# Kernel tuning notes

Hardware: AMD Instinct MI355X
Metric: run time of the kernel (lower is better)

## Reference

```python
import jax, jax.numpy as jnp
import numpy as np

N = 750_000      # total nodes (10,000 graphs x 75 superpixels)
E = 6_000_000    # directed edges (avg degree 8)
G = 10_000       # number of graphs
NINP, H, HFC, NCLS = 2, 64, 32, 10
BN_EPS = 1e-5


def setup_inputs() -> dict:
    key = jax.random.key(0)
    ks = jax.random.split(key, 12)
    x = jax.random.normal(ks[0], (N, NINP), dtype=jnp.float32)
    edge_index = jax.random.randint(ks[1], (2, E), 0, N, dtype=jnp.int32)
    batch = jnp.sort(jax.random.randint(ks[2], (N,), 0, G, dtype=jnp.int32))
    def glorot(k, shape):
        fan_in, fan_out = shape
        s = jnp.sqrt(6.0 / (fan_in + fan_out)).astype(jnp.float32)
        return jax.random.uniform(k, shape, jnp.float32, -s, s)
    return {
        "x": x, "edge_index": edge_index, "batch": batch,
        "W1": glorot(ks[3], (NINP, H)), "b1": jnp.zeros((H,), jnp.float32),
        "W2": glorot(ks[4], (H, H)),    "b2": jnp.zeros((H,), jnp.float32),
        "W3": glorot(ks[5], (H, H)),    "b3": jnp.zeros((H,), jnp.float32),
        "gamma": jnp.ones((H,), jnp.float32), "beta": jnp.zeros((H,), jnp.float32),
        "fcW1": glorot(ks[6], (H, HFC)),  "fcb1": jnp.zeros((HFC,), jnp.float32),
        "fcW2": glorot(ks[7], (HFC, NCLS)), "fcb2": jnp.zeros((NCLS,), jnp.float32),
    }


def reference(x, edge_index, batch, W1, b1, W2, b2, W3, b3,
              gamma, beta, fcW1, fcb1, fcW2, fcb2):
    n = x.shape[0]
    loop = jnp.arange(n, dtype=edge_index.dtype)
    src = jnp.concatenate([edge_index[0], loop])   # [E+N] self-loops added
    dst = jnp.concatenate([edge_index[1], loop])
    # symmetric GCN normalization: deg from destination with unit edge weights
    deg = jax.ops.segment_sum(jnp.ones_like(dst, jnp.float32), dst, num_segments=n)
    dinv = jnp.where(deg > 0, jax.lax.rsqrt(deg), 0.0)
    norm = (dinv[src] * dinv[dst])[:, None]        # [E+N, 1]

    def gcn_conv(h, W, b):
        h = h @ W                                   # linear transform first (small K)
        msg = h[src] * norm                         # gather + normalize
        return jax.ops.segment_sum(msg, dst, num_segments=n) + b  # scatter-add

    h = jax.nn.relu(gcn_conv(x, W1, b1))
    h = jax.nn.relu(gcn_conv(h, W2, b2))
    h = jax.nn.relu(gcn_conv(h, W3, b3))

    # global mean pool over graphs
    sums = jax.ops.segment_sum(h, batch, num_segments=G)
    cnts = jax.ops.segment_sum(jnp.ones((n, 1), jnp.float32), batch, num_segments=G)
    pooled = sums / jnp.maximum(cnts, 1.0)          # [G, H]

    # BatchNorm1d (training mode: batch statistics, biased variance)
    mean = pooled.mean(axis=0)
    var = pooled.var(axis=0)
    hbn = (pooled - mean) * jax.lax.rsqrt(var + BN_EPS) * gamma + beta

    h = jax.nn.relu(hbn @ fcW1 + fcb1)
    logits = h @ fcW2 + fcb2
    return jax.nn.log_softmax(logits, axis=1)
```

## Files before the change

kernel.cpp:

```cpp
#include <hip/hip_runtime.h>
#include <hip/hip_fp16.h>

#define HDIM 64
#define HFC 32
#define NCLS 10
#define DT32 32

#define NBUCK 256
#define BSH   12
#define BUCKN 4096
#define EPT   16
#define CHUNK 4096
#define CAPSH 16
#define CAP   (1 << CAPSH)

__device__ inline __half2 u2h2(unsigned int u) {
    __half2 r;
    *reinterpret_cast<unsigned int*>(&r) = u;
    return r;
}
__device__ inline unsigned int h22u(__half2 h) {
    return *reinterpret_cast<unsigned int*>(&h);
}

__device__ inline float fdot2u(unsigned int a, unsigned int b, float c) {
#if __has_builtin(__builtin_amdgcn_fdot2)
    typedef _Float16 f16x2 __attribute__((ext_vector_type(2)));
    union U { unsigned int u; f16x2 h; };
    U ua, ub; ua.u = a; ub.u = b;
    return __builtin_amdgcn_fdot2(ua.h, ub.h, c, false);
#else
    float2 fa = __half22float2(u2h2(a));
    float2 fb = __half22float2(u2h2(b));
    return fmaf(fa.x, fb.x, fmaf(fa.y, fb.y, c));
#endif
}


__global__ void k_initcur(int* __restrict__ gcur) {
    gcur[threadIdx.x] = threadIdx.x << CAPSH;
}

__global__ __launch_bounds__(256) void k_split(const int* __restrict__ src,
                                               const int* __restrict__ dst,
                                               int* __restrict__ gcur,
                                               unsigned int* __restrict__ part, int E) {
    __shared__ int cnt[NBUCK];
    __shared__ int off[NBUCK];
    cnt[threadIdx.x] = 0;
    __syncthreads();
    int base = blockIdx.x * CHUNK + threadIdx.x;
    int s16[EPT], d16[EPT], b16[EPT];
    #pragma unroll
    for (int i = 0; i < EPT; ++i) {
        int e = base + i * 256;
        bool ok = e < E;
        s16[i] = ok ? src[e] : 0;
        d16[i] = ok ? dst[e] : 0;
        b16[i] = ok ? (d16[i] >> BSH) : -1;
        if (ok) atomicAdd(&cnt[b16[i]], 1);
    }
    __syncthreads();
    {
        int c = cnt[threadIdx.x];
        off[threadIdx.x] = c ? atomicAdd(&gcur[threadIdx.x], c) : 0;
    }
    __syncthreads();
    #pragma unroll
    for (int i = 0; i < EPT; ++i) {
        if (b16[i] >= 0) {
            int slot = atomicAdd(&off[b16[i]], 1);
            part[slot] = ((unsigned)(d16[i] & (BUCKN - 1)) << 20) | (unsigned)s16[i];
        }
    }
}

__global__ __launch_bounds__(256) void k_build(const unsigned int* __restrict__ part,
                                               const int* __restrict__ gcur,
                                               unsigned int* __restrict__ begdeg,
                                               int* __restrict__ col, int n) {
    __shared__ int cnt[BUCKN];
    __shared__ int tmp[256];
    const int b = blockIdx.x;
    const int s = b << CAPSH, t = gcur[b];
    const int nodeBase = b << BSH;
    for (int i = threadIdx.x; i < BUCKN; i += 256) cnt[i] = 0;
    __syncthreads();
    for (int e = s + threadIdx.x; e < t; e += 256) {
        int local = (int)(part[e] >> 20);
        atomicAdd(&cnt[local], 1);
    }
    __syncthreads();
    int my[16]; int sum = 0;
    #pragma unroll
    for (int i = 0; i < 16; ++i) { my[i] = cnt[threadIdx.x * 16 + i]; sum += my[i]; }
    tmp[threadIdx.x] = sum; __syncthreads();
    for (int o = 1; o < 256; o <<= 1) {
        int v = ((int)threadIdx.x >= o) ? tmp[threadIdx.x - o] : 0;
        __syncthreads();
        tmp[threadIdx.x] += v;
        __syncthreads();
    }
    int run = tmp[threadIdx.x] - sum + s;
    __syncthreads();
    #pragma unroll
    for (int i = 0; i < 16; ++i) {
        int local = threadIdx.x * 16 + i;
        int node = nodeBase + local;
        int c = my[i];
        cnt[local] = run;
        if (node < n) begdeg[node] = ((unsigned)c << 24) | (unsigned)run;
        run += c;
    }
    __syncthreads();
    for (int e = s + threadIdx.x; e < t; e += 256) {
        unsigned int pe = part[e];
        int local = (int)(pe >> 20);
        int p = atomicAdd(&cnt[local], 1);
        col[p] = (int)(pe & 0xFFFFFu);
    }
}


__global__ void k_xs(const float* __restrict__ x, const unsigned int* __restrict__ begdeg,
                     unsigned int* __restrict__ xsh, int n) {
    int i = blockIdx.x * blockDim.x + threadIdx.x;
    if (i >= n) return;
    unsigned int bd = begdeg[i];
    float dv = rsqrtf((float)(bd >> 24) + 1.0f);
    float2 v = reinterpret_cast<const float2*>(x)[i];
    xsh[i] = h22u(__floats2half2_rn(v.x * dv, v.y * dv));
}

__global__ void k_gather1(const unsigned int* __restrict__ begdeg, const int* __restrict__ col,
                          const unsigned int* __restrict__ xsh,
                          uint2* __restrict__ aggd, int n) {
    int d = blockIdx.x * blockDim.x + threadIdx.x;
    if (d >= n) return;
    unsigned int bd = begdeg[d];
    int e0 = (int)(bd & 0xFFFFFFu);
    int deg = (int)(bd >> 24);
    int e1 = e0 + deg;
    float dv = rsqrtf((float)deg + 1.0f);
    float2 v = __half22float2(u2h2(xsh[d]));
    float a0 = v.x, a1 = v.y;
    for (int e = e0; e < e1; ++e) {
        float2 w = __half22float2(u2h2(xsh[col[e]]));
        a0 += w.x; a1 += w.y;
    }
    uint2 o;
    o.x = h22u(__floats2half2_rn(a0 * dv, a1 * dv));
    o.y = h22u(__floats2half2_rn(dv, 0.0f));
    aggd[d] = o;
}

__global__ __launch_bounds__(256) void k_layer12(
        const unsigned int* __restrict__ begdeg, const int* __restrict__ col,
        const uint2* __restrict__ aggd,
        const float* __restrict__ W1, const float* __restrict__ b1,
        const float* __restrict__ W2, const float* __restrict__ b2,
        __half* __restrict__ out, int n) {
    __shared__ unsigned int sWp[HDIM / 2][HDIM];
    __shared__ float sB2[HDIM];
    __shared__ float sW1a[HDIM], sW1b[HDIM], sB1[HDIM];
    __shared__ unsigned int sAgg[DT32][HDIM / 2];
    __shared__ __half sOut[DT32][HDIM];

    for (int i = threadIdx.x; i < (HDIM / 2) * HDIM; i += 256) {
        int k2 = i >> 6, f = i & 63;
        sWp[k2][f] = h22u(__floats2half2_rn(W2[(2 * k2) * HDIM + f], W2[(2 * k2 + 1) * HDIM + f]));
    }
    if (threadIdx.x < HDIM) {
        sW1a[threadIdx.x] = W1[threadIdx.x];
        sW1b[threadIdx.x] = W1[HDIM + threadIdx.x];
        sB1[threadIdx.x] = b1[threadIdx.x];
        sB2[threadIdx.x] = b2[threadIdx.x];
    }
    __syncthreads();

    const int base = blockIdx.x * DT32;
    const int nValid = min(DT32, n - base);
    const int nd = threadIdx.x >> 3;
    const int q  = threadIdx.x & 7;
    const int node = base + nd;

    float w1a[8], w1b[8], bb[8];
    #pragma unroll
    for (int j = 0; j < 8; ++j) {
        int f = q * 8 + j;
        w1a[j] = sW1a[f]; w1b[j] = sW1b[f]; bb[j] = sB1[f];
    }

    float selfdv = 1.0f;
    if (nd < nValid) {
        float acc[8];
        uint2 sv = aggd[node];
        float2 z = __half22float2(u2h2(sv.x));
        selfdv = __half22float2(u2h2(sv.y)).x;
        #pragma unroll
        for (int j = 0; j < 8; ++j)
            acc[j] = fmaxf(fmaf(z.x, w1a[j], fmaf(z.y, w1b[j], bb[j])), 0.0f) * selfdv;
        unsigned int bd = begdeg[node];
        int e0 = (int)(bd & 0xFFFFFFu);
        int e1 = e0 + (int)(bd >> 24);
        int e = e0;
        for (; e + 4 <= e1; e += 4) {
            int c0 = col[e], c1 = col[e + 1], c2 = col[e + 2], c3 = col[e + 3];
            uint2 v0 = aggd[c0];
            uint2 v1 = aggd[c1];
            uint2 v2 = aggd[c2];
            uint2 v3 = aggd[c3];
            float2 z0 = __half22float2(u2h2(v0.x)); float d0 = __half22float2(u2h2(v0.y)).x;
            float2 z1 = __half22float2(u2h2(v1.x)); float d1 = __half22float2(u2h2(v1.y)).x;
            float2 z2 = __half22float2(u2h2(v2.x)); float d2 = __half22float2(u2h2(v2.y)).x;
            float2 z3 = __half22float2(u2h2(v3.x)); float d3 = __half22float2(u2h2(v3.y)).x;
            #pragma unroll
            for (int j = 0; j < 8; ++j) {
                acc[j] = fmaf(fmaxf(fmaf(z0.x, w1a[j], fmaf(z0.y, w1b[j], bb[j])), 0.0f), d0, acc[j]);
                acc[j] = fmaf(fmaxf(fmaf(z1.x, w1a[j], fmaf(z1.y, w1b[j], bb[j])), 0.0f), d1, acc[j]);
                acc[j] = fmaf(fmaxf(fmaf(z2.x, w1a[j], fmaf(z2.y, w1b[j], bb[j])), 0.0f), d2, acc[j]);
                acc[j] = fmaf(fmaxf(fmaf(z3.x, w1a[j], fmaf(z3.y, w1b[j], bb[j])), 0.0f), d3, acc[j]);
            }
        }
        for (; e < e1; ++e) {
            uint2 v0 = aggd[col[e]];
            float2 z0 = __half22float2(u2h2(v0.x)); float d0 = __half22float2(u2h2(v0.y)).x;
            #pragma unroll
            for (int j = 0; j < 8; ++j)
                acc[j] = fmaf(fmaxf(fmaf(z0.x, w1a[j], fmaf(z0.y, w1b[j], bb[j])), 0.0f), d0, acc[j]);
        }
        uint4 o;
        o.x = h22u(__floats2half2_rn(acc[0] * selfdv, acc[1] * selfdv));
        o.y = h22u(__floats2half2_rn(acc[2] * selfdv, acc[3] * selfdv));
        o.z = h22u(__floats2half2_rn(acc[4] * selfdv, acc[5] * selfdv));
        o.w = h22u(__floats2half2_rn(acc[6] * selfdv, acc[7] * selfdv));
        *reinterpret_cast<uint4*>(&sAgg[nd][q * 4]) = o;
    }
    __syncthreads();

    {
        const int f  = threadIdx.x & 63;
        const int ng = threadIdx.x >> 6;
        for (int ii = ng; ii < DT32; ii += 4) {
            int onode = base + ii;
            if (onode >= n) break;
            float acc = sB2[f];
            #pragma unroll
            for (int k2 = 0; k2 < HDIM / 2; ++k2)
                acc = fdot2u(sAgg[ii][k2], sWp[k2][f], acc);
            unsigned int bd = begdeg[onode];
            float sc = rsqrtf((float)(bd >> 24) + 1.0f);
            sOut[ii][f] = __float2half(fmaxf(acc, 0.0f) * sc);
        }
    }
    __syncthreads();

    if (nd < nValid) {
        uint4 o = reinterpret_cast<const uint4*>(&sOut[0][0])[nd * 8 + q];
        reinterpret_cast<uint4*>(out)[(long long)node * 8 + q] = o;
    }
}

__global__ __launch_bounds__(256) void k_layer64(
        const unsigned int* __restrict__ begdeg, const int* __restrict__ col,
        const __half* __restrict__ hs,
        const float* __restrict__ W, const float* __restrict__ b,
        const int* __restrict__ batchArr,
        float* __restrict__ pooled, int n) {
    __shared__ unsigned int sWp[HDIM / 2][HDIM];
    __shared__ float sB[HDIM];
    __shared__ unsigned int sAgg[DT32][HDIM / 2];
    __shared__ __half sOut[DT32][HDIM];
    __shared__ int sGid[DT32];

    for (int i = threadIdx.x; i < (HDIM / 2) * HDIM; i += 256) {
        int k2 = i >> 6, f = i & 63;
        sWp[k2][f] = h22u(__floats2half2_rn(W[(2 * k2) * HDIM + f], W[(2 * k2 + 1) * HDIM + f]));
    }
    if (threadIdx.x < HDIM) sB[threadIdx.x] = b[threadIdx.x];

    const int base = blockIdx.x * DT32;
    const int nValid = min(DT32, n - base);
    const int nd = threadIdx.x >> 3;
    const int q  = threadIdx.x & 7;
    const int node = base + nd;

    if (threadIdx.x < DT32)
        sGid[threadIdx.x] = (threadIdx.x < nValid) ? batchArr[base + threadIdx.x] : -1;

    if (nd < nValid) {
        const uint4* rows = reinterpret_cast<const uint4*>(hs);
        uint4 v = rows[(long long)node * 8 + q];
        __half2 a0 = u2h2(v.x), a1 = u2h2(v.y), a2 = u2h2(v.z), a3 = u2h2(v.w);
        __half2 b0 = u2h2(0u), b1 = u2h2(0u), b2 = u2h2(0u), b3 = u2h2(0u);
        unsigned int bd = begdeg[node];
        int e0 = (int)(bd & 0xFFFFFFu);
        int deg = (int)(bd >> 24);
        int e1 = e0 + deg;
        int e = e0;
        for (; e + 8 <= e1; e += 8) {
            int c0 = col[e], c1 = col[e + 1], c2 = col[e + 2], c3 = col[e + 3];
            int c4 = col[e + 4], c5 = col[e + 5], c6 = col[e + 6], c7 = col[e + 7];
            uint4 w0 = rows[(long long)c0 * 8 + q];
            uint4 w1 = rows[(long long)c1 * 8 + q];
            uint4 w2 = rows[(long long)c2 * 8 + q];
            uint4 w3 = rows[(long long)c3 * 8 + q];
            uint4 w4 = rows[(long long)c4 * 8 + q];
            uint4 w5 = rows[(long long)c5 * 8 + q];
            uint4 w6 = rows[(long long)c6 * 8 + q];
            uint4 w7 = rows[(long long)c7 * 8 + q];
            a0 = __hadd2(a0, u2h2(w0.x)); a1 = __hadd2(a1, u2h2(w0.y));
            a2 = __hadd2(a2, u2h2(w0.z)); a3 = __hadd2(a3, u2h2(w0.w));
            b0 = __hadd2(b0, u2h2(w1.x)); b1 = __hadd2(b1, u2h2(w1.y));
            b2 = __hadd2(b2, u2h2(w1.z)); b3 = __hadd2(b3, u2h2(w1.w));
            a0 = __hadd2(a0, u2h2(w2.x)); a1 = __hadd2(a1, u2h2(w2.y));
            a2 = __hadd2(a2, u2h2(w2.z)); a3 = __hadd2(a3, u2h2(w2.w));
            b0 = __hadd2(b0, u2h2(w3.x)); b1 = __hadd2(b1, u2h2(w3.y));
            b2 = __hadd2(b2, u2h2(w3.z)); b3 = __hadd2(b3, u2h2(w3.w));
            a0 = __hadd2(a0, u2h2(w4.x)); a1 = __hadd2(a1, u2h2(w4.y));
            a2 = __hadd2(a2, u2h2(w4.z)); a3 = __hadd2(a3, u2h2(w4.w));
            b0 = __hadd2(b0, u2h2(w5.x)); b1 = __hadd2(b1, u2h2(w5.y));
            b2 = __hadd2(b2, u2h2(w5.z)); b3 = __hadd2(b3, u2h2(w5.w));
            a0 = __hadd2(a0, u2h2(w6.x)); a1 = __hadd2(a1, u2h2(w6.y));
            a2 = __hadd2(a2, u2h2(w6.z)); a3 = __hadd2(a3, u2h2(w6.w));
            b0 = __hadd2(b0, u2h2(w7.x)); b1 = __hadd2(b1, u2h2(w7.y));
            b2 = __hadd2(b2, u2h2(w7.z)); b3 = __hadd2(b3, u2h2(w7.w));
        }
        for (; e + 4 <= e1; e += 4) {
            int c0 = col[e], c1 = col[e + 1], c2 = col[e + 2], c3 = col[e + 3];
            uint4 w0 = rows[(long long)c0 * 8 + q];
            uint4 w1 = rows[(long long)c1 * 8 + q];
            uint4 w2 = rows[(long long)c2 * 8 + q];
            uint4 w3 = rows[(long long)c3 * 8 + q];
            a0 = __hadd2(a0, u2h2(w0.x)); a1 = __hadd2(a1, u2h2(w0.y));
            a2 = __hadd2(a2, u2h2(w0.z)); a3 = __hadd2(a3, u2h2(w0.w));
            b0 = __hadd2(b0, u2h2(w1.x)); b1 = __hadd2(b1, u2h2(w1.y));
            b2 = __hadd2(b2, u2h2(w1.z)); b3 = __hadd2(b3, u2h2(w1.w));
            a0 = __hadd2(a0, u2h2(w2.x)); a1 = __hadd2(a1, u2h2(w2.y));
            a2 = __hadd2(a2, u2h2(w2.z)); a3 = __hadd2(a3, u2h2(w2.w));
            b0 = __hadd2(b0, u2h2(w3.x)); b1 = __hadd2(b1, u2h2(w3.y));
            b2 = __hadd2(b2, u2h2(w3.z)); b3 = __hadd2(b3, u2h2(w3.w));
        }
        for (; e < e1; ++e) {
            uint4 w = rows[(long long)col[e] * 8 + q];
            a0 = __hadd2(a0, u2h2(w.x)); a1 = __hadd2(a1, u2h2(w.y));
            a2 = __hadd2(a2, u2h2(w.z)); a3 = __hadd2(a3, u2h2(w.w));
        }
        a0 = __hadd2(a0, b0); a1 = __hadd2(a1, b1);
        a2 = __hadd2(a2, b2); a3 = __hadd2(a3, b3);
        float dv = rsqrtf((float)deg + 1.0f);
        float2 f0 = __half22float2(a0), f1 = __half22float2(a1);
        float2 f2 = __half22float2(a2), f3 = __half22float2(a3);
        uint4 o;
        o.x = h22u(__floats2half2_rn(f0.x * dv, f0.y * dv));
        o.y = h22u(__floats2half2_rn(f1.x * dv, f1.y * dv));
        o.z = h22u(__floats2half2_rn(f2.x * dv, f2.y * dv));
        o.w = h22u(__floats2half2_rn(f3.x * dv, f3.y * dv));
        *reinterpret_cast<uint4*>(&sAgg[nd][q * 4]) = o;
    }
    __syncthreads();

    {
        const int f  = threadIdx.x & 63;
        const int ng = threadIdx.x >> 6;
        for (int ii = ng; ii < DT32; ii += 4) {
            int onode = base + ii;
            if (onode >= n) break;
            float acc = sB[f];
            #pragma unroll
            for (int k2 = 0; k2 < HDIM / 2; ++k2)
                acc = fdot2u(sAgg[ii][k2], sWp[k2][f], acc);
            sOut[ii][f] = __float2half(fmaxf(acc, 0.0f));
        }
    }
    __syncthreads();

    if (threadIdx.x < HDIM) {
        int f = threadIdx.x;
        float acc = 0.0f;
        int prev = sGid[0];
        for (int ii = 0; ii < nValid; ++ii) {
            int g = sGid[ii];
            if (g != prev) {
                if (prev >= 0) atomicAdd(&pooled[(long long)prev * HDIM + f], acc);
                acc = 0.0f; prev = g;
            }
            acc += __half2float(sOut[ii][f]);
        }
        if (prev >= 0) atomicAdd(&pooled[(long long)prev * HDIM + f], acc);
    }
}


__global__ void k_start(const int* __restrict__ batch, int* __restrict__ startArr,
                        int n, int G) {
    int g = blockIdx.x * blockDim.x + threadIdx.x;
    if (g > G) return;
    int lo = 0, hi = n;
    while (lo < hi) {
        int mid = (lo + hi) >> 1;
        if (batch[mid] < g) lo = mid + 1; else hi = mid;
    }
    startArr[g] = lo;
}

__global__ void k_bnstats(const float* __restrict__ pooled, const int* __restrict__ startArr,
                          const float* __restrict__ gamma, const float* __restrict__ beta,
                          float* __restrict__ scale, float* __restrict__ shift, int G) {
    int f = blockIdx.x;
    __shared__ float ss[256], ss2[256];
    float s = 0.0f, s2 = 0.0f;
    for (int g = threadIdx.x; g < G; g += blockDim.x) {
        float c = (float)(startArr[g + 1] - startArr[g]);
        float v = pooled[(long long)g * HDIM + f] / fmaxf(c, 1.0f);
        s += v; s2 += v * v;
    }
    ss[threadIdx.x] = s; ss2[threadIdx.x] = s2;
    __syncthreads();
    for (int off = 128; off > 0; off >>= 1) {
        if (threadIdx.x < off) {
            ss[threadIdx.x]  += ss[threadIdx.x + off];
            ss2[threadIdx.x] += ss2[threadIdx.x + off];
        }
        __syncthreads();
    }
    if (threadIdx.x == 0) {
        float mean = ss[0] / (float)G;
        float var  = ss2[0] / (float)G - mean * mean;
        float rstd = rsqrtf(var + 1e-5f);
        float sc = gamma[f] * rstd;
        scale[f] = sc;
        shift[f] = beta[f] - mean * sc;
    }
}

__global__ void k_head(const float* __restrict__ pooled, const int* __restrict__ startArr,
                       const float* __restrict__ scale, const float* __restrict__ shift,
                       const float* __restrict__ fcW1, const float* __restrict__ fcb1,
                       const float* __restrict__ fcW2, const float* __restrict__ fcb2,
                       float* __restrict__ out, int G) {
    __shared__ float sW1[HDIM * HFC];
    __shared__ float sW2[HFC * NCLS];
    __shared__ float sb1[HFC], sb2[NCLS], ssc[HDIM], ssh[HDIM];
    for (int i = threadIdx.x; i < HDIM * HFC; i += blockDim.x) sW1[i] = fcW1[i];
    for (int i = threadIdx.x; i < HFC * NCLS; i += blockDim.x) sW2[i] = fcW2[i];
    if (threadIdx.x < HFC)  sb1[threadIdx.x] = fcb1[threadIdx.x];
    if (threadIdx.x < NCLS) sb2[threadIdx.x] = fcb2[threadIdx.x];
    if (threadIdx.x < HDIM) { ssc[threadIdx.x] = scale[threadIdx.x]; ssh[threadIdx.x] = shift[threadIdx.x]; }
    __syncthreads();
    int g = blockIdx.x * blockDim.x + threadIdx.x;
    if (g >= G) return;
    float inv = 1.0f / fmaxf((float)(startArr[g + 1] - startArr[g]), 1.0f);
    float bn[HDIM];
    #pragma unroll
    for (int f = 0; f < HDIM; ++f)
        bn[f] = pooled[(long long)g * HDIM + f] * inv * ssc[f] + ssh[f];
    float hfc[HFC];
    #pragma unroll
    for (int j = 0; j < HFC; ++j) {
        float a = sb1[j];
        #pragma unroll
        for (int f = 0; f < HDIM; ++f) a = fmaf(bn[f], sW1[f * HFC + j], a);
        hfc[j] = fmaxf(a, 0.0f);
    }
    float lg[NCLS];
    float mx = -1e30f;
    #pragma unroll
    for (int c = 0; c < NCLS; ++c) {
        float a = sb2[c];
        #pragma unroll
        for (int j = 0; j < HFC; ++j) a = fmaf(hfc[j], sW2[j * NCLS + c], a);
        lg[c] = a;
        mx = fmaxf(mx, a);
    }
    float se = 0.0f;
    #pragma unroll
    for (int c = 0; c < NCLS; ++c) se += expf(lg[c] - mx);
    float lse = mx + logf(se);
    #pragma unroll
    for (int c = 0; c < NCLS; ++c) out[(long long)g * NCLS + c] = lg[c] - lse;
}


static inline char* bump(char*& p, size_t bytes) {
    char* r = p;
    p += (bytes + 255) & ~(size_t)255;
    return r;
}

extern "C" void kernel_launch(void* const* d_in, const int* in_sizes, int n_in,
                              void* d_out, int out_size, void* d_ws, size_t ws_size,
                              hipStream_t stream) {
    const float* x     = (const float*)d_in[0];
    const int*   ei    = (const int*)d_in[1];
    const int*   batch = (const int*)d_in[2];
    const float* W1    = (const float*)d_in[3];
    const float* b1    = (const float*)d_in[4];
    const float* W2    = (const float*)d_in[5];
    const float* b2    = (const float*)d_in[6];
    const float* W3    = (const float*)d_in[7];
    const float* b3    = (const float*)d_in[8];
    const float* gamma = (const float*)d_in[9];
    const float* beta  = (const float*)d_in[10];
    const float* fcW1  = (const float*)d_in[11];
    const float* fcb1  = (const float*)d_in[12];
    const float* fcW2  = (const float*)d_in[13];
    const float* fcb2  = (const float*)d_in[14];

    const long long n = in_sizes[2];
    const int ni = (int)n;
    const int E = in_sizes[1] / 2;
    const int G = out_size / NCLS;
    const int* src = ei;
    const int* dst = ei + E;
    const int B = 256;

    char* p = (char*)d_ws;
    int*          gcur   = (int*)bump(p, NBUCK * 4);
    unsigned int* begdeg = (unsigned int*)bump(p, n * 4);
    int*          startA = (int*)bump(p, (size_t)(G + 1) * 4);
    float*        pooled = (float*)bump(p, (size_t)G * HDIM * 4);
    float*        scale  = (float*)bump(p, 2 * HDIM * 4);
    float*        shift  = scale + HDIM;
    unsigned int* xsh    = (unsigned int*)bump(p, n * 4);
    uint2*        aggd   = (uint2*)bump(p, (size_t)n * 8);
    char*         R      = bump(p, (size_t)HDIM * n * 2);
    int*          col    = (int*)bump(p, (size_t)NBUCK * CAP * 4);

    unsigned int* part = (unsigned int*)R;
    __half* hB = (__half*)R;

    (void)hipMemsetAsync(pooled, 0, (size_t)G * HDIM * 4, stream);

    const int nchunk = (E + CHUNK - 1) / CHUNK;
    const int nbU = (ni + BUCKN - 1) >> BSH;
    k_initcur<<<1, NBUCK, 0, stream>>>(gcur);
    k_split<<<nchunk, B, 0, stream>>>(src, dst, gcur, part, E);
    k_build<<<nbU, B, 0, stream>>>(part, gcur, begdeg, col, ni);

    k_start<<<(G + 1 + B - 1) / B, B, 0, stream>>>(batch, startA, ni, G);

    k_xs<<<(ni + B - 1) / B, B, 0, stream>>>(x, begdeg, xsh, ni);
    k_gather1<<<(ni + B - 1) / B, B, 0, stream>>>(begdeg, col, xsh, aggd, ni);

    const int nblk = (ni + DT32 - 1) / DT32;
    k_layer12<<<nblk, B, 0, stream>>>(begdeg, col, aggd, W1, b1, W2, b2, hB, ni);

    k_layer64<<<nblk, B, 0, stream>>>(begdeg, col, hB, W3, b3, batch, pooled, ni);

    k_bnstats<<<HDIM, B, 0, stream>>>(pooled, startA, gamma, beta, scale, shift, G);
    k_head<<<(G + B - 1) / B, B, 0, stream>>>(pooled, startA, scale, shift,
                                              fcW1, fcb1, fcW2, fcb2, (float*)d_out, G);
}
```

Before: 610.7 us.

## Use packed half math in layer12 with 64 nodes per block; unroll gather1

The fused layer1/layer2 kernel now computes the recomputed layer-1 activations and accumulates neighbor messages with packed fp16 FMAs and a packed-max ReLU instead of fp32 math. Each thread handles 16 features, so a 256-thread block covers 64 nodes and the weight setup is amortized over more nodes, halving the grid. The gather1 edge loop is unrolled by four to issue more independent loads. Accumulating in fp16 raises rounding error, and the wider per-thread work cuts the number of threads available to hide gather latency.

```diff
diff --git a/kernel.cpp b/kernel.cpp
--- a/kernel.cpp
+++ b/kernel.cpp
@@ -5,6 +5,7 @@
 #define HFC 32
 #define NCLS 10
 #define DT32 32
+#define DT64 64
 
 #define NBUCK 256
 #define BSH   12
@@ -21,6 +22,12 @@
 }
 __device__ inline unsigned int h22u(__half2 h) {
     return *reinterpret_cast<unsigned int*>(&h);
+}
+
+__device__ inline __half2 h2relu(__half2 a) {
+    unsigned int ua = h22u(a), uz = 0u, r;
+    asm("v_pk_max_f16 %0, %1, %2" : "=v"(r) : "v"(ua), "v"(uz));
+    return u2h2(r);
 }
 
 __device__ inline float fdot2u(unsigned int a, unsigned int b, float c) {
@@ -144,7 +151,17 @@
     float dv = rsqrtf((float)deg + 1.0f);
     float2 v = __half22float2(u2h2(xsh[d]));
     float a0 = v.x, a1 = v.y;
-    for (int e = e0; e < e1; ++e) {
+    int e = e0;
+    for (; e + 4 <= e1; e += 4) {
+        int c0 = col[e], c1 = col[e + 1], c2 = col[e + 2], c3 = col[e + 3];
+        float2 w0 = __half22float2(u2h2(xsh[c0]));
+        float2 w1 = __half22float2(u2h2(xsh[c1]));
+        float2 w2 = __half22float2(u2h2(xsh[c2]));
+        float2 w3 = __half22float2(u2h2(xsh[c3]));
+        a0 += w0.x + w1.x + w2.x + w3.x;
+        a1 += w0.y + w1.y + w2.y + w3.y;
+    }
+    for (; e < e1; ++e) {
         float2 w = __half22float2(u2h2(xsh[col[e]]));
         a0 += w.x; a1 += w.y;
     }
@@ -163,8 +180,8 @@
     __shared__ unsigned int sWp[HDIM / 2][HDIM];
     __shared__ float sB2[HDIM];
     __shared__ float sW1a[HDIM], sW1b[HDIM], sB1[HDIM];
-    __shared__ unsigned int sAgg[DT32][HDIM / 2];
-    __shared__ __half sOut[DT32][HDIM];
+    __shared__ unsigned int sAgg[DT64][HDIM / 2];
+    __shared__ __half sOut[DT64][HDIM];
 
     for (int i = threadIdx.x; i < (HDIM / 2) * HDIM; i += 256) {
         int k2 = i >> 6, f = i & 63;
@@ -178,28 +195,32 @@
     }
     __syncthreads();
 
-    const int base = blockIdx.x * DT32;
-    const int nValid = min(DT32, n - base);
-    const int nd = threadIdx.x >> 3;
-    const int q  = threadIdx.x & 7;
+    const int base = blockIdx.x * DT64;
+    const int nValid = min(DT64, n - base);
+    const int nd = threadIdx.x >> 2;
+    const int q  = threadIdx.x & 3;
     const int node = base + nd;
 
-    float w1a[8], w1b[8], bb[8];
+    __half2 w1a2[8], w1b2[8], bb2[8];
     #pragma unroll
     for (int j = 0; j < 8; ++j) {
-        int f = q * 8 + j;
-        w1a[j] = sW1a[f]; w1b[j] = sW1b[f]; bb[j] = sB1[f];
-    }
-
-    float selfdv = 1.0f;
+        int f = q * 16 + 2 * j;
+        w1a2[j] = __floats2half2_rn(sW1a[f], sW1a[f + 1]);
+        w1b2[j] = __floats2half2_rn(sW1b[f], sW1b[f + 1]);
+        bb2[j]  = __floats2half2_rn(sB1[f], sB1[f + 1]);
+    }
+
     if (nd < nValid) {
-        float acc[8];
+        __half2 acc[8];
         uint2 sv = aggd[node];
-        float2 z = __half22float2(u2h2(sv.x));
-        selfdv = __half22float2(u2h2(sv.y)).x;
+        __half2 zz = u2h2(sv.x);
+        __half2 zx2 = __low2half2(zz), zy2 = __high2half2(zz);
+        __half2 sd2 = __low2half2(u2h2(sv.y));
         #pragma unroll
-        for (int j = 0; j < 8; ++j)
-            acc[j] = fmaxf(fmaf(z.x, w1a[j], fmaf(z.y, w1b[j], bb[j])), 0.0f) * selfdv;
+        for (int j = 0; j < 8; ++j) {
+            __half2 t = __hfma2(zx2, w1a2[j], __hfma2(zy2, w1b2[j], bb2[j]));
+            acc[j] = __hmul2(h2relu(t), sd2);
+        }
         unsigned int bd = begdeg[node];
         int e0 = (int)(bd & 0xFFFFFFu);
         int e1 = e0 + (int)(bd >> 24);
@@ -210,38 +231,47 @@
             uint2 v1 = aggd[c1];
             uint2 v2 = aggd[c2];
             uint2 v3 = aggd[c3];
-            float2 z0 = __half22float2(u2h2(v0.x)); float d0 = __half22float2(u2h2(v0.y)).x;
-            float2 z1 = __half22float2(u2h2(v1.x)); float d1 = __half22float2(u2h2(v1.y)).x;
-            float2 z2 = __half22float2(u2h2(v2.x)); float d2 = __half22float2(u2h2(v2.y)).x;
-            float2 z3 = __half22float2(u2h2(v3.x)); float d3 = __half22float2(u2h2(v3.y)).x;
+            __half2 z0 = u2h2(v0.x), z1 = u2h2(v1.x), z2 = u2h2(v2.x), z3 = u2h2(v3.x);
+            __half2 x0 = __low2half2(z0), y0 = __high2half2(z0), d0 = __low2half2(u2h2(v0.y));
+            __half2 x1 = __low2half2(z1), y1 = __high2half2(z1), d1 = __low2half2(u2h2(v1.y));
+            __half2 x2 = __low2half2(z2), y2 = __high2half2(z2), d2 = __low2half2(u2h2(v2.y));
+            __half2 x3 = __low2half2(z3), y3 = __high2half2(z3), d3 = __low2half2(u2h2(v3.y));
             #pragma unroll
             for (int j = 0; j < 8; ++j) {
-                acc[j] = fmaf(fmaxf(fmaf(z0.x, w1a[j], fmaf(z0.y, w1b[j], bb[j])), 0.0f), d0, acc[j]);
-                acc[j] = fmaf(fmaxf(fmaf(z1.x, w1a[j], fmaf(z1.y, w1b[j], bb[j])), 0.0f), d1, acc[j]);
-                acc[j] = fmaf(fmaxf(fmaf(z2.x, w1a[j], fmaf(z2.y, w1b[j], bb[j])), 0.0f), d2, acc[j]);
-                acc[j] = fmaf(fmaxf(fmaf(z3.x, w1a[j], fmaf(z3.y, w1b[j], bb[j])), 0.0f), d3, acc[j]);
+                __half2 t0 = __hfma2(x0, w1a2[j], __hfma2(y0, w1b2[j], bb2[j]));
+                acc[j] = __hfma2(h2relu(t0), d0, acc[j]);
+                __half2 t1 = __hfma2(x1, w1a2[j], __hfma2(y1, w1b2[j], bb2[j]));
+                acc[j] = __hfma2(h2relu(t1), d1, acc[j]);
+                __half2 t2 = __hfma2(x2, w1a2[j], __hfma2(y2, w1b2[j], bb2[j]));
+                acc[j] = __hfma2(h2relu(t2), d2, acc[j]);
+                __half2 t3 = __hfma2(x3, w1a2[j], __hfma2(y3, w1b2[j], bb2[j]));
+                acc[j] = __hfma2(h2relu(t3), d3, acc[j]);
             }
         }
         for (; e < e1; ++e) {
             uint2 v0 = aggd[col[e]];
-            float2 z0 = __half22float2(u2h2(v0.x)); float d0 = __half22float2(u2h2(v0.y)).x;
+            __half2 z0 = u2h2(v0.x);
+            __half2 x0 = __low2half2(z0), y0 = __high2half2(z0), d0 = __low2half2(u2h2(v0.y));
             #pragma unroll
-            for (int j = 0; j < 8; ++j)
-                acc[j] = fmaf(fmaxf(fmaf(z0.x, w1a[j], fmaf(z0.y, w1b[j], bb[j])), 0.0f), d0, acc[j]);
-        }
-        uint4 o;
-        o.x = h22u(__floats2half2_rn(acc[0] * selfdv, acc[1] * selfdv));
-        o.y = h22u(__floats2half2_rn(acc[2] * selfdv, acc[3] * selfdv));
-        o.z = h22u(__floats2half2_rn(acc[4] * selfdv, acc[5] * selfdv));
-        o.w = h22u(__floats2half2_rn(acc[6] * selfdv, acc[7] * selfdv));
-        *reinterpret_cast<uint4*>(&sAgg[nd][q * 4]) = o;
+            for (int j = 0; j < 8; ++j) {
+                __half2 t0 = __hfma2(x0, w1a2[j], __hfma2(y0, w1b2[j], bb2[j]));
+                acc[j] = __hfma2(h2relu(t0), d0, acc[j]);
+            }
+        }
+        #pragma unroll
+        for (int j = 0; j < 8; ++j) acc[j] = __hmul2(acc[j], sd2);
+        uint4 o0, o1;
+        o0.x = h22u(acc[0]); o0.y = h22u(acc[1]); o0.z = h22u(acc[2]); o0.w = h22u(acc[3]);
+        o1.x = h22u(acc[4]); o1.y = h22u(acc[5]); o1.z = h22u(acc[6]); o1.w = h22u(acc[7]);
+        uint4* sa = reinterpret_cast<uint4*>(&sAgg[nd][q * 8]);
+        sa[0] = o0; sa[1] = o1;
     }
     __syncthreads();
 
     {
         const int f  = threadIdx.x & 63;
         const int ng = threadIdx.x >> 6;
-        for (int ii = ng; ii < DT32; ii += 4) {
+        for (int ii = ng; ii < DT64; ii += 4) {
             int onode = base + ii;
             if (onode >= n) break;
             float acc = sB2[f];
@@ -256,8 +286,10 @@
     __syncthreads();
 
     if (nd < nValid) {
-        uint4 o = reinterpret_cast<const uint4*>(&sOut[0][0])[nd * 8 + q];
-        reinterpret_cast<uint4*>(out)[(long long)node * 8 + q] = o;
+        const uint4* so = reinterpret_cast<const uint4*>(&sOut[nd][q * 16]);
+        uint4* go = reinterpret_cast<uint4*>(out + (long long)node * HDIM + q * 16);
+        go[0] = so[0];
+        go[1] = so[1];
     }
 }
 
@@ -543,10 +575,11 @@
     k_xs<<<(ni + B - 1) / B, B, 0, stream>>>(x, begdeg, xsh, ni);
     k_gather1<<<(ni + B - 1) / B, B, 0, stream>>>(begdeg, col, xsh, aggd, ni);
 
-    const int nblk = (ni + DT32 - 1) / DT32;
-    k_layer12<<<nblk, B, 0, stream>>>(begdeg, col, aggd, W1, b1, W2, b2, hB, ni);
-
-    k_layer64<<<nblk, B, 0, stream>>>(begdeg, col, hB, W3, b3, batch, pooled, ni);
+    const int nblk64 = (ni + DT64 - 1) / DT64;
+    k_layer12<<<nblk64, B, 0, stream>>>(begdeg, col, aggd, W1, b1, W2, b2, hB, ni);
+
+    const int nblk32 = (ni + DT32 - 1) / DT32;
+    k_layer64<<<nblk32, B, 0, stream>>>(begdeg, col, hB, W3, b3, batch, pooled, ni);
 
     k_bnstats<<<HDIM, B, 0, stream>>>(pooled, startA, gamma, beta, scale, shift, G);
     k_head<<<(G + B - 1) / B, B, 0, stream>>>(pooled, startA, scale, shift,
```

New measurement: 581.1 us. -4.8%, faster.
